# Performance work log

Hardware: AMD Instinct MI355X
Metric: run time of the kernel (lower is better)

## Reference

```python
import jax, jax.numpy as jnp
import numpy as np

EPS = 1e-5
K = 20

def knn_idx(x, k):
    # x: (B, C, N); returns indices of k nearest neighbors (incl. self), (B, N, k)
    xx = jnp.sum(x * x, axis=1, keepdims=True)            # (B,1,N)
    inner = -2.0 * jnp.einsum('bcn,bcm->bnm', x, x)       # (B,N,N)
    d = -jnp.swapaxes(xx, 1, 2) - inner - xx              # -||xi - xj||^2
    return jax.lax.top_k(d, k)[1]

def graph_feature(x, k):
    # x: (B, C, N) -> (B, 2C, N, k) with [neighbor - center, center]
    B, C, N = x.shape
    idx = knn_idx(x, k)                                   # (B,N,k)
    feat = jnp.swapaxes(x, 1, 2)                          # (B,N,C)
    nb = jax.vmap(lambda f, i: f[i])(feat, idx)           # (B,N,k,C) gather
    ctr = jnp.broadcast_to(feat[:, :, None, :], nb.shape)
    out = jnp.concatenate([nb - ctr, ctr], axis=-1)       # (B,N,k,2C)
    return jnp.transpose(out, (0, 3, 1, 2))

def bn(x, g, b, m, v):
    # inference-mode batchnorm over channel axis 1
    shape = (1, -1) + (1,) * (x.ndim - 2)
    inv = g / jnp.sqrt(v + EPS)
    return x * inv.reshape(shape) + (b - m * inv).reshape(shape)

def edge_block(x, W, g, b, m, v):
    f = graph_feature(x, K)                               # (B,2C,N,k)
    h = jnp.einsum('bcnk,oc->bonk', f, W)                 # 1x1 conv, no bias
    h = jax.nn.relu(bn(h, g, b, m, v))
    return jnp.max(h, axis=-1)                            # max over k -> (B,O,N)

def _forward(x, W1, W2, W3, W4, W5,
             g1, b1, m1, v1, g2, b2, m2, v2, g3, b3, m3, v3,
             g4, b4, m4, v4, g5, b5, m5, v5, g6, b6, m6, v6,
             g7, b7, m7, v7, L1W, L2W, L2b, L3W, L3b):
    x1 = edge_block(x, W1, g1, b1, m1, v1)                # (B,64,N)
    x2 = edge_block(x1, W2, g2, b2, m2, v2)               # (B,64,N)
    x3 = edge_block(x2, W3, g3, b3, m3, v3)               # (B,128,N)
    x4 = edge_block(x3, W4, g4, b4, m4, v4)               # (B,256,N)
    cat = jnp.concatenate([x1, x2, x3, x4], axis=1)       # (B,512,N)
    h = jnp.einsum('bcn,oc->bon', cat, W5)                # conv5 1x1
    h = jax.nn.relu(bn(h, g5, b5, m5, v5))
    h = jnp.max(h, axis=-1)                               # adaptive max pool -> (B,1024)
    h = jax.nn.relu(bn(h @ L1W.T, g6, b6, m6, v6))        # dropout = identity (eval)
    h = jax.nn.relu(bn(h @ L2W.T + L2b, g7, b7, m7, v7))
    return h @ L3W.T + L3b                                # (B, num_classes)

def _bn_params(keys, c):
    k0, k1, k2, k3 = keys
    g = jax.random.uniform(k0, (c,), jnp.float32, 0.5, 1.5)
    b = 0.1 * jax.random.normal(k1, (c,), jnp.float32)
    m = 0.1 * jax.random.normal(k2, (c,), jnp.float32)
    v = jax.random.uniform(k3, (c,), jnp.float32, 0.5, 1.5)
    return g, b, m, v

def setup_inputs() -> dict:
    key = jax.random.key(0)
    ks = jax.random.split(key, 40)
    d = {}
    d['x'] = jax.random.normal(ks[0], (8, 4, 1024), jnp.float32)
    def w(k, o, i):
        return jax.random.normal(k, (o, i), jnp.float32) * np.float32(np.sqrt(2.0 / i))
    d['W1'] = w(ks[1], 64, 8)
    d['W2'] = w(ks[2], 64, 128)
    d['W3'] = w(ks[3], 128, 128)
    d['W4'] = w(ks[4], 256, 256)
    d['W5'] = w(ks[5], 1024, 512)
    for i, c in enumerate([64, 64, 128, 256, 1024, 512, 256]):
        g, b, m, v = _bn_params(jax.random.split(ks[6 + i], 4), c)
        d[f'g{i+1}'], d[f'b{i+1}'], d[f'm{i+1}'], d[f'v{i+1}'] = g, b, m, v
    d['L1W'] = w(ks[20], 512, 1024)
    d['L2W'] = w(ks[21], 256, 512)
    d['L2b'] = 0.1 * jax.random.normal(ks[22], (256,), jnp.float32)
    d['L3W'] = w(ks[23], 8, 256)
    d['L3b'] = 0.1 * jax.random.normal(ks[24], (8,), jnp.float32)
    return d

def reference(x, W1, W2, W3, W4, W5,
              g1, b1, m1, v1, g2, b2, m2, v2, g3, b3, m3, v3,
              g4, b4, m4, v4, g5, b5, m5, v5, g6, b6, m6, v6,
              g7, b7, m7, v7, L1W, L2W, L2b, L3W, L3b):
    return _forward(x, W1, W2, W3, W4, W5,
                    g1, b1, m1, v1, g2, b2, m2, v2, g3, b3, m3, v3,
                    g4, b4, m4, v4, g5, b5, m5, v5, g6, b6, m6, v6,
                    g7, b7, m7, v7, L1W, L2W, L2b, L3W, L3b)
```

## Files before the change

kernel.cpp:

```cpp
#include <hip/hip_runtime.h>
#include <cstdint>

#define BB 8
#define NN 1024
#define KK 20
#define EPSV 1e-5f

typedef __attribute__((ext_vector_type(8))) short bf16x8;
typedef __attribute__((ext_vector_type(4))) float f32x4;

__device__ __forceinline__ unsigned fenc(float f) {
  unsigned u = __float_as_uint(f);
  return (u & 0x80000000u) ? ~u : (u | 0x80000000u);
}
__device__ __forceinline__ float fdec(unsigned u) {
  u = (u & 0x80000000u) ? (u & 0x7FFFFFFFu) : ~u;
  return __uint_as_float(u);
}
__device__ __forceinline__ unsigned short f2bf(float f) {
  unsigned u = __float_as_uint(f);
  unsigned r = u + 0x7FFFu + ((u >> 16) & 1u);
  return (unsigned short)(r >> 16);
}

template<int C>
__global__ __launch_bounds__(256) void xx_kernel(const float* __restrict__ x, float* __restrict__ xx) {
  int p = blockIdx.x * 256 + threadIdx.x;
  if (p >= BB * NN) return;
  int b = p >> 10, n = p & (NN - 1);
  const float* xb = x + (size_t)b * C * NN + n;
  float s = 0.f;
  #pragma unroll
  for (int c = 0; c < C; ++c) { float t = xb[(size_t)c * NN]; s = fmaf(t, t, s); }
  xx[p] = s;
}

template<int C>
__global__ __launch_bounds__(256) void dist_kernel(const float* __restrict__ x, const float* __restrict__ xx,
                                                   float* __restrict__ d, int b0) {
  constexpr int CC = (C < 32) ? C : 32;
  __shared__ __align__(16) float xi[CC][128];
  __shared__ __align__(16) float xj[CC][128];
  int bl = blockIdx.z, b = b0 + bl;
  int i0 = blockIdx.y * 128, j0 = blockIdx.x * 128;
  int t = threadIdx.x;
  int w = t >> 6, lane = t & 63;
  int wi = (w >> 1) * 64, wj = (w & 1) * 64;
  int li = (lane >> 3) * 8, lj = (lane & 7) * 8;
  float acc[8][8] = {};
  const float* xb = x + (size_t)b * C * NN;
  for (int c0 = 0; c0 < C; c0 += CC) {
    __syncthreads();
    for (int p = t; p < CC * 32; p += 256) {
      int cc = p >> 5, col = (p & 31) * 4;
      *reinterpret_cast<float4*>(&xi[cc][col]) =
        *reinterpret_cast<const float4*>(&xb[(size_t)(c0 + cc) * NN + i0 + col]);
      *reinterpret_cast<float4*>(&xj[cc][col]) =
        *reinterpret_cast<const float4*>(&xb[(size_t)(c0 + cc) * NN + j0 + col]);
    }
    __syncthreads();
    #pragma unroll
    for (int cc = 0; cc < CC; ++cc) {
      float4 A0 = *reinterpret_cast<const float4*>(&xi[cc][wi + li]);
      float4 A1 = *reinterpret_cast<const float4*>(&xi[cc][wi + li + 4]);
      float4 B0 = *reinterpret_cast<const float4*>(&xj[cc][wj + lj]);
      float4 B1 = *reinterpret_cast<const float4*>(&xj[cc][wj + lj + 4]);
      float av[8] = {A0.x, A0.y, A0.z, A0.w, A1.x, A1.y, A1.z, A1.w};
      float bv[8] = {B0.x, B0.y, B0.z, B0.w, B1.x, B1.y, B1.z, B1.w};
      #pragma unroll
      for (int a = 0; a < 8; ++a)
        #pragma unroll
        for (int q = 0; q < 8; ++q)
          acc[a][q] = fmaf(av[a], bv[q], acc[a][q]);
    }
  }
  float xxj[8];
  #pragma unroll
  for (int q = 0; q < 8; ++q) xxj[q] = xx[b * NN + j0 + wj + lj + q];
  #pragma unroll
  for (int a = 0; a < 8; ++a) {
    int i = i0 + wi + li + a;
    float xxi = xx[b * NN + i];
    float4 o0v, o1v;
    o0v.x = 2.f * acc[a][0] - xxi - xxj[0];
    o0v.y = 2.f * acc[a][1] - xxi - xxj[1];
    o0v.z = 2.f * acc[a][2] - xxi - xxj[2];
    o0v.w = 2.f * acc[a][3] - xxi - xxj[3];
    o1v.x = 2.f * acc[a][4] - xxi - xxj[4];
    o1v.y = 2.f * acc[a][5] - xxi - xxj[5];
    o1v.z = 2.f * acc[a][6] - xxi - xxj[6];
    o1v.w = 2.f * acc[a][7] - xxi - xxj[7];
    *reinterpret_cast<float4*>(&d[((size_t)bl * NN + i) * NN + j0 + wj + lj]) = o0v;
    *reinterpret_cast<float4*>(&d[((size_t)bl * NN + i) * NN + j0 + wj + lj + 4]) = o1v;
  }
}

__global__ __launch_bounds__(256) void topk_kernel(const float* __restrict__ d, int* __restrict__ idx, int b0) {
  int t = threadIdx.x;
  int wave = t >> 6, lane = t & 63;
  int bl = blockIdx.y, b = b0 + bl;
  int i = blockIdx.x * 4 + wave;
  const float* row = d + ((size_t)bl * NN + i) * NN;

  unsigned v[16];
  #pragma unroll
  for (int p = 0; p < 4; ++p) {
    float4 f = *reinterpret_cast<const float4*>(&row[p * 256 + lane * 4]);
    v[p * 4 + 0] = fenc(f.x);
    v[p * 4 + 1] = fenc(f.y);
    v[p * 4 + 2] = fenc(f.z);
    v[p * 4 + 3] = fenc(f.w);
  }

  unsigned long long lo = 0, hi = 0xFFFFFFFFull;
  while (lo < hi) {
    unsigned long long mid = lo + ((hi - lo + 1) >> 1);
    unsigned mt = (unsigned)mid;
    int c = 0;
    #pragma unroll
    for (int e = 0; e < 16; ++e)
      c += __popcll(__ballot(v[e] >= mt));
    if (c >= KK) lo = mid; else hi = mid - 1;
  }
  unsigned T = (unsigned)lo;

  int* op = idx + ((size_t)b * NN + i) * KK;
  int base = 0, n1 = 0;
  #pragma unroll
  for (int e = 0; e < 16; ++e) {
    unsigned long long mask = __ballot(v[e] > T);
    unsigned mb = __builtin_amdgcn_mbcnt_lo((unsigned)mask, 0u);
    mb = __builtin_amdgcn_mbcnt_hi((unsigned)(mask >> 32), mb);
    if (v[e] > T) op[base + mb] = (e >> 2) * 256 + lane * 4 + (e & 3);
    base += __popcll(mask);
  }
  n1 = base;
  int need = KK - n1;
  int neq = 0;
  #pragma unroll
  for (int e = 0; e < 16; ++e) neq += __popcll(__ballot(v[e] == T));
  if (neq == need) {
    #pragma unroll
    for (int e = 0; e < 16; ++e) {
      unsigned long long mask = __ballot(v[e] == T);
      unsigned mb = __builtin_amdgcn_mbcnt_lo((unsigned)mask, 0u);
      mb = __builtin_amdgcn_mbcnt_hi((unsigned)(mask >> 32), mb);
      if (v[e] == T) op[base + mb] = (e >> 2) * 256 + lane * 4 + (e & 3);
      base += __popcll(mask);
    }
  } else {
    unsigned taken = 0;
    for (int s = 0; s < need; ++s) {
      int jm = 1 << 30;
      #pragma unroll
      for (int e = 0; e < 16; ++e) {
        if (v[e] == T && !((taken >> e) & 1u)) {
          int j = (e >> 2) * 256 + lane * 4 + (e & 3);
          jm = jm < j ? jm : j;
        }
      }
      #pragma unroll
      for (int st = 1; st < 64; st <<= 1) {
        int oj = __shfl_xor(jm, st);
        jm = jm < oj ? jm : oj;
      }
      if (lane == ((jm >> 2) & 63)) {
        int e = (((jm >> 8) << 2) | (jm & 3));
        taken |= 1u << e;
        op[base + s] = jm;
      }
    }
  }
}

template<int C, int O>
__global__ __launch_bounds__(256) void pgemm_kernel(const float* __restrict__ x, const float* __restrict__ W,
                                                    float* __restrict__ Plo, float* __restrict__ Phi) {
  constexpr int CC = (C < 64) ? C : 64;
  __shared__ __align__(16) float xs[CC][64];
  __shared__ __align__(16) float wls[CC][68];
  __shared__ __align__(16) float whs[CC][68];
  int b = blockIdx.z;
  int o0 = blockIdx.y * 64, n0 = blockIdx.x * 64;
  int t = threadIdx.x;
  int tn = t & 15, to = t >> 4;
  float accl[4][4] = {}, acch[4][4] = {};
  const float* xb = x + (size_t)b * C * NN;
  for (int c0 = 0; c0 < C; c0 += CC) {
    __syncthreads();
    for (int p = t; p < CC * 64; p += 256) {
      int cc = p >> 6, col = p & 63;
      xs[cc][col] = xb[(size_t)(c0 + cc) * NN + n0 + col];
    }
    for (int p = t; p < 64 * CC; p += 256) {
      int ol = p / CC, cc = p % CC;
      wls[cc][ol] = W[(size_t)(o0 + ol) * (2 * C) + c0 + cc];
      whs[cc][ol] = W[(size_t)(o0 + ol) * (2 * C) + C + c0 + cc];
    }
    __syncthreads();
    #pragma unroll
    for (int cc = 0; cc < CC; ++cc) {
      float4 X  = *reinterpret_cast<const float4*>(&xs[cc][tn * 4]);
      float4 Wl = *reinterpret_cast<const float4*>(&wls[cc][to * 4]);
      float4 Wh = *reinterpret_cast<const float4*>(&whs[cc][to * 4]);
      float xv[4] = {X.x, X.y, X.z, X.w};
      float wl[4] = {Wl.x, Wl.y, Wl.z, Wl.w};
      float wh[4] = {Wh.x, Wh.y, Wh.z, Wh.w};
      #pragma unroll
      for (int a = 0; a < 4; ++a)
        #pragma unroll
        for (int q = 0; q < 4; ++q) {
          accl[a][q] = fmaf(wl[a], xv[q], accl[a][q]);
          acch[a][q] = fmaf(wh[a], xv[q], acch[a][q]);
        }
    }
  }
  #pragma unroll
  for (int a = 0; a < 4; ++a) {
    int o = o0 + to * 4 + a;
    size_t base = ((size_t)b * O + o) * NN + n0 + tn * 4;
    float4 vl = {accl[a][0], accl[a][1], accl[a][2], accl[a][3]};
    float4 vh = {acch[a][0], acch[a][1], acch[a][2], acch[a][3]};
    *reinterpret_cast<float4*>(&Plo[base]) = vl;
    *reinterpret_cast<float4*>(&Phi[base]) = vh;
  }
}

__global__ __launch_bounds__(256) void edgemax_kernel(const float* __restrict__ Plo, const float* __restrict__ Phi,
    const int* __restrict__ idx, const float* __restrict__ g, const float* __restrict__ bt,
    const float* __restrict__ m, const float* __restrict__ v,
    float* __restrict__ xout, int O) {
  __shared__ __align__(16) float srow[2][NN];
  __shared__ __align__(16) float sphi[2][64];
  __shared__ int   sidx[64 * KK];
  __shared__ float sinv[32], ssb[32];
  int b = blockIdx.z, n0 = blockIdx.y * 64, o0 = blockIdx.x * 32;
  int t = threadIdx.x;
  if (t < 32) {
    float inv = g[o0 + t] / sqrtf(v[o0 + t] + EPSV);
    sinv[t] = inv; ssb[t] = bt[o0 + t] - m[o0 + t] * inv;
  }
  for (int p = t; p < 64 * KK; p += 256) sidx[p] = idx[((size_t)b * NN + n0) * KK + p];
  const float* plobase = Plo + (size_t)b * O * NN;
  const float* phibase = Phi + (size_t)b * O * NN;
  float4 cur0 = *reinterpret_cast<const float4*>(&plobase[(size_t)(o0 + 0) * NN + t * 4]);
  float4 cur1 = *reinterpret_cast<const float4*>(&plobase[(size_t)(o0 + 1) * NN + t * 4]);
  float4 curphi;
  if (t < 32) curphi = *reinterpret_cast<const float4*>(&phibase[(size_t)(o0 + (t >> 4)) * NN + n0 + (t & 15) * 4]);
  __syncthreads();
  int n = t >> 2, kg = t & 3;
  int j0 = sidx[n * KK + kg * 5 + 0];
  int j1 = sidx[n * KK + kg * 5 + 1];
  int j2 = sidx[n * KK + kg * 5 + 2];
  int j3 = sidx[n * KK + kg * 5 + 3];
  int j4 = sidx[n * KK + kg * 5 + 4];
  for (int oo = 0; oo < 32; oo += 2) {
    *reinterpret_cast<float4*>(&srow[0][t * 4]) = cur0;
    *reinterpret_cast<float4*>(&srow[1][t * 4]) = cur1;
    if (t < 32) *reinterpret_cast<float4*>(&sphi[t >> 4][(t & 15) * 4]) = curphi;
    if (oo < 30) {
      cur0 = *reinterpret_cast<const float4*>(&plobase[(size_t)(o0 + oo + 2) * NN + t * 4]);
      cur1 = *reinterpret_cast<const float4*>(&plobase[(size_t)(o0 + oo + 3) * NN + t * 4]);
      if (t < 32) curphi = *reinterpret_cast<const float4*>(&phibase[(size_t)(o0 + oo + 2 + (t >> 4)) * NN + n0 + (t & 15) * 4]);
    }
    __syncthreads();
    float mx0 = srow[0][j0];
    mx0 = fmaxf(mx0, srow[0][j1]);
    mx0 = fmaxf(mx0, srow[0][j2]);
    mx0 = fmaxf(mx0, srow[0][j3]);
    mx0 = fmaxf(mx0, srow[0][j4]);
    float mx1 = srow[1][j0];
    mx1 = fmaxf(mx1, srow[1][j1]);
    mx1 = fmaxf(mx1, srow[1][j2]);
    mx1 = fmaxf(mx1, srow[1][j3]);
    mx1 = fmaxf(mx1, srow[1][j4]);
    mx0 = fmaxf(mx0, __shfl_xor(mx0, 1));
    mx0 = fmaxf(mx0, __shfl_xor(mx0, 2));
    mx1 = fmaxf(mx1, __shfl_xor(mx1, 1));
    mx1 = fmaxf(mx1, __shfl_xor(mx1, 2));
    if (kg == 0) {
      float z0 = mx0 - srow[0][n0 + n] + sphi[0][n];
      float z1 = mx1 - srow[1][n0 + n] + sphi[1][n];
      xout[((size_t)b * O + o0 + oo) * NN + n0 + n]     = fmaxf(fmaf(z0, sinv[oo],     ssb[oo]),     0.f);
      xout[((size_t)b * O + o0 + oo + 1) * NN + n0 + n] = fmaxf(fmaf(z1, sinv[oo + 1], ssb[oo + 1]), 0.f);
    }
    __syncthreads();
  }
}

__global__ __launch_bounds__(256) void tcvt_kernel(const float* __restrict__ src,
    unsigned short* __restrict__ dst, int Csrc, int c0) {
  __shared__ float tile[64][65];
  int b = blockIdx.z, cb = blockIdx.y * 64, n0 = blockIdx.x * 64;
  int t = threadIdx.x;
  const float* s = src + ((size_t)b * Csrc + cb) * NN + n0;
  #pragma unroll
  for (int rr = 0; rr < 4; ++rr) {
    int r = (t >> 4) + rr * 16;
    float4 v = *reinterpret_cast<const float4*>(&s[(size_t)r * NN + (t & 15) * 4]);
    tile[r][(t & 15) * 4 + 0] = v.x;
    tile[r][(t & 15) * 4 + 1] = v.y;
    tile[r][(t & 15) * 4 + 2] = v.z;
    tile[r][(t & 15) * 4 + 3] = v.w;
  }
  __syncthreads();
  #pragma unroll
  for (int rr = 0; rr < 2; ++rr) {
    int chunk = t + 256 * rr;
    int n = chunk >> 3, cg = (chunk & 7) * 8;
    unsigned short u[8];
    #pragma unroll
    for (int j = 0; j < 8; ++j) u[j] = f2bf(tile[cg + j][n]);
    *reinterpret_cast<uint4*>(&dst[((size_t)b * NN + n0 + n) * 512 + c0 + cb + cg]) =
      *reinterpret_cast<const uint4*>(u);
  }
}

__global__ __launch_bounds__(256) void cvtw_kernel(const float* __restrict__ W, unsigned short* __restrict__ Wb) {
  int p = (blockIdx.x * 256 + threadIdx.x) * 4;
  float4 v = *reinterpret_cast<const float4*>(&W[p]);
  unsigned short u[4] = {f2bf(v.x), f2bf(v.y), f2bf(v.z), f2bf(v.w)};
  *reinterpret_cast<uint2*>(&Wb[p]) = *reinterpret_cast<const uint2*>(u);
}

__global__ __launch_bounds__(256) void pgemm4_mfma_kernel(const unsigned short* __restrict__ Xb,
    const unsigned short* __restrict__ W4b, float* __restrict__ Plo_t, float* __restrict__ Phi_t) {
  int b = blockIdx.z;
  int n0 = blockIdx.x * 128, o0 = blockIdx.y * 64;
  int t = threadIdx.x, lane = t & 63, w = t >> 6;
  int r = lane & 15, kc = lane >> 4;
  const unsigned short* A  = Xb + ((size_t)b * NN + n0 + w * 32 + r) * 512 + 128 + kc * 8;
  const unsigned short* Bw = W4b + ((size_t)(o0 + r)) * 256 + kc * 8;
  f32x4 accl0[4] = {}, accl1[4] = {}, acch0[4] = {}, acch1[4] = {};
  #pragma unroll
  for (int ks = 0; ks < 128; ks += 32) {
    bf16x8 a0 = *reinterpret_cast<const bf16x8*>(A + ks);
    bf16x8 a1 = *reinterpret_cast<const bf16x8*>(A + 16 * 512 + ks);
    #pragma unroll
    for (int j = 0; j < 4; ++j) {
      bf16x8 bl = *reinterpret_cast<const bf16x8*>(Bw + (size_t)j * 16 * 256 + ks);
      bf16x8 bh = *reinterpret_cast<const bf16x8*>(Bw + (size_t)j * 16 * 256 + 128 + ks);
      accl0[j] = __builtin_amdgcn_mfma_f32_16x16x32_bf16(a0, bl, accl0[j], 0, 0, 0);
      accl1[j] = __builtin_amdgcn_mfma_f32_16x16x32_bf16(a1, bl, accl1[j], 0, 0, 0);
      acch0[j] = __builtin_amdgcn_mfma_f32_16x16x32_bf16(a0, bh, acch0[j], 0, 0, 0);
      acch1[j] = __builtin_amdgcn_mfma_f32_16x16x32_bf16(a1, bh, acch1[j], 0, 0, 0);
    }
  }
  #pragma unroll
  for (int j = 0; j < 4; ++j) {
    #pragma unroll
    for (int reg = 0; reg < 4; ++reg) {
      size_t n_a = (size_t)b * NN + n0 + w * 32 + kc * 4 + reg;
      size_t n_b = n_a + 16;
      int oc = o0 + j * 16 + r;
      Plo_t[n_a * 256 + oc] = accl0[j][reg];
      Plo_t[n_b * 256 + oc] = accl1[j][reg];
      Phi_t[n_a * 256 + oc] = acch0[j][reg];
      Phi_t[n_b * 256 + oc] = acch1[j][reg];
    }
  }
}

__global__ __launch_bounds__(256) void edgemax4_kernel(const float* __restrict__ Plo_t,
    const float* __restrict__ Phi_t, const int* __restrict__ idx,
    const float* __restrict__ g, const float* __restrict__ bt,
    const float* __restrict__ m, const float* __restrict__ v,
    unsigned short* __restrict__ Xb) {
  int b = blockIdx.y, t = threadIdx.x;
  int n = blockIdx.x * 4 + (t >> 6);
  int oc = (t & 63) * 4;
  const int* ip = idx + ((size_t)b * NN + n) * KK;
  const float* base = Plo_t + (size_t)b * NN * 256;
  float4 mx = {-3.4e38f, -3.4e38f, -3.4e38f, -3.4e38f};
  #pragma unroll
  for (int k = 0; k < KK; ++k) {
    float4 vv = *reinterpret_cast<const float4*>(base + (size_t)ip[k] * 256 + oc);
    mx.x = fmaxf(mx.x, vv.x);
    mx.y = fmaxf(mx.y, vv.y);
    mx.z = fmaxf(mx.z, vv.z);
    mx.w = fmaxf(mx.w, vv.w);
  }
  float4 self = *reinterpret_cast<const float4*>(base + (size_t)n * 256 + oc);
  float4 ph = *reinterpret_cast<const float4*>(Phi_t + ((size_t)b * NN + n) * 256 + oc);
  float4 gg = *reinterpret_cast<const float4*>(g + oc);
  float4 bb = *reinterpret_cast<const float4*>(bt + oc);
  float4 mm = *reinterpret_cast<const float4*>(m + oc);
  float4 vv4 = *reinterpret_cast<const float4*>(v + oc);
  float mxa[4] = {mx.x, mx.y, mx.z, mx.w};
  float sfa[4] = {self.x, self.y, self.z, self.w};
  float pha[4] = {ph.x, ph.y, ph.z, ph.w};
  float ga[4] = {gg.x, gg.y, gg.z, gg.w};
  float ba[4] = {bb.x, bb.y, bb.z, bb.w};
  float ma[4] = {mm.x, mm.y, mm.z, mm.w};
  float va[4] = {vv4.x, vv4.y, vv4.z, vv4.w};
  unsigned short u[4];
  #pragma unroll
  for (int e = 0; e < 4; ++e) {
    float inv = ga[e] / sqrtf(va[e] + EPSV);
    float z = mxa[e] - sfa[e] + pha[e];
    float y = fmaxf(fmaf(z, inv, ba[e] - ma[e] * inv), 0.f);
    u[e] = f2bf(y);
  }
  *reinterpret_cast<uint2*>(&Xb[((size_t)b * NN + n) * 512 + 256 + oc]) =
    *reinterpret_cast<const uint2*>(u);
}

__global__ __launch_bounds__(256) void conv5_mfma_kernel(const unsigned short* __restrict__ Xb,
    const unsigned short* __restrict__ W5b, unsigned* __restrict__ henc) {
  int b = blockIdx.z;
  int n0 = blockIdx.x * 128, o0 = blockIdx.y * 64;
  int t = threadIdx.x, lane = t & 63, w = t >> 6;
  int r = lane & 15, kc = lane >> 4;
  const unsigned short* A = W5b + ((size_t)(o0 + r)) * 512 + kc * 8;
  const unsigned short* B = Xb + ((size_t)b * NN + n0 + w * 32 + r) * 512 + kc * 8;
  f32x4 acc00 = {}, acc01 = {}, acc10 = {}, acc11 = {};
  f32x4 acc20 = {}, acc21 = {}, acc30 = {}, acc31 = {};
  bf16x8 a0 = *reinterpret_cast<const bf16x8*>(A + 0 * 16 * 512);
  bf16x8 a1 = *reinterpret_cast<const bf16x8*>(A + 1 * 16 * 512);
  bf16x8 a2 = *reinterpret_cast<const bf16x8*>(A + 2 * 16 * 512);
  bf16x8 a3 = *reinterpret_cast<const bf16x8*>(A + 3 * 16 * 512);
  bf16x8 b0 = *reinterpret_cast<const bf16x8*>(B);
  bf16x8 b1 = *reinterpret_cast<const bf16x8*>(B + 16 * 512);
  #pragma unroll
  for (int ks = 0; ks < 512; ks += 32) {
    bf16x8 na0, na1, na2, na3, nb0, nb1;
    if (ks + 32 < 512) {
      na0 = *reinterpret_cast<const bf16x8*>(A + 0 * 16 * 512 + ks + 32);
      na1 = *reinterpret_cast<const bf16x8*>(A + 1 * 16 * 512 + ks + 32);
      na2 = *reinterpret_cast<const bf16x8*>(A + 2 * 16 * 512 + ks + 32);
      na3 = *reinterpret_cast<const bf16x8*>(A + 3 * 16 * 512 + ks + 32);
      nb0 = *reinterpret_cast<const bf16x8*>(B + ks + 32);
      nb1 = *reinterpret_cast<const bf16x8*>(B + 16 * 512 + ks + 32);
    }
    acc00 = __builtin_amdgcn_mfma_f32_16x16x32_bf16(a0, b0, acc00, 0, 0, 0);
    acc01 = __builtin_amdgcn_mfma_f32_16x16x32_bf16(a0, b1, acc01, 0, 0, 0);
    acc10 = __builtin_amdgcn_mfma_f32_16x16x32_bf16(a1, b0, acc10, 0, 0, 0);
    acc11 = __builtin_amdgcn_mfma_f32_16x16x32_bf16(a1, b1, acc11, 0, 0, 0);
    acc20 = __builtin_amdgcn_mfma_f32_16x16x32_bf16(a2, b0, acc20, 0, 0, 0);
    acc21 = __builtin_amdgcn_mfma_f32_16x16x32_bf16(a2, b1, acc21, 0, 0, 0);
    acc30 = __builtin_amdgcn_mfma_f32_16x16x32_bf16(a3, b0, acc30, 0, 0, 0);
    acc31 = __builtin_amdgcn_mfma_f32_16x16x32_bf16(a3, b1, acc31, 0, 0, 0);
    a0 = na0; a1 = na1; a2 = na2; a3 = na3; b0 = nb0; b1 = nb1;
  }
  f32x4 m0 = {fmaxf(acc00[0], acc01[0]), fmaxf(acc00[1], acc01[1]),
              fmaxf(acc00[2], acc01[2]), fmaxf(acc00[3], acc01[3])};
  f32x4 m1 = {fmaxf(acc10[0], acc11[0]), fmaxf(acc10[1], acc11[1]),
              fmaxf(acc10[2], acc11[2]), fmaxf(acc10[3], acc11[3])};
  f32x4 m2 = {fmaxf(acc20[0], acc21[0]), fmaxf(acc20[1], acc21[1]),
              fmaxf(acc20[2], acc21[2]), fmaxf(acc20[3], acc21[3])};
  f32x4 m3 = {fmaxf(acc30[0], acc31[0]), fmaxf(acc30[1], acc31[1]),
              fmaxf(acc30[2], acc31[2]), fmaxf(acc30[3], acc31[3])};
  #pragma unroll
  for (int st = 1; st < 16; st <<= 1) {
    #pragma unroll
    for (int reg = 0; reg < 4; ++reg) {
      m0[reg] = fmaxf(m0[reg], __shfl_xor(m0[reg], st));
      m1[reg] = fmaxf(m1[reg], __shfl_xor(m1[reg], st));
      m2[reg] = fmaxf(m2[reg], __shfl_xor(m2[reg], st));
      m3[reg] = fmaxf(m3[reg], __shfl_xor(m3[reg], st));
    }
  }
  if (r == 0) {
    #pragma unroll
    for (int reg = 0; reg < 4; ++reg) {
      atomicMax(&henc[b * 1024 + o0 + 0 * 16 + kc * 4 + reg], fenc(m0[reg]));
      atomicMax(&henc[b * 1024 + o0 + 1 * 16 + kc * 4 + reg], fenc(m1[reg]));
      atomicMax(&henc[b * 1024 + o0 + 2 * 16 + kc * 4 + reg], fenc(m2[reg]));
      atomicMax(&henc[b * 1024 + o0 + 3 * 16 + kc * 4 + reg], fenc(m3[reg]));
    }
  }
}

__global__ __launch_bounds__(256) void fc1_kernel(
    const unsigned* __restrict__ henc,
    const float* __restrict__ g5, const float* __restrict__ b5, const float* __restrict__ m5, const float* __restrict__ v5,
    const float* __restrict__ L1W,
    const float* __restrict__ g6, const float* __restrict__ b6, const float* __restrict__ m6, const float* __restrict__ v6,
    float* __restrict__ y1) {
  __shared__ float sh[1024];
  int b = blockIdx.y, t = threadIdx.x;
  int o0 = blockIdx.x * 64;
  for (int o = t; o < 1024; o += 256) {
    float f = fdec(henc[b * 1024 + o]);
    float inv = g5[o] / sqrtf(v5[o] + EPSV);
    sh[o] = fmaxf(fmaf(f, inv, b5[o] - m5[o] * inv), 0.f);
  }
  __syncthreads();
  int o = o0 + (t >> 2), part = t & 3;
  float acc = 0.f;
  const float4* w4 = reinterpret_cast<const float4*>(L1W + (size_t)o * 1024 + part * 256);
  const float4* h4 = reinterpret_cast<const float4*>(sh + part * 256);
  #pragma unroll 8
  for (int c = 0; c < 64; ++c) {
    float4 a = w4[c], q = h4[c];
    acc = fmaf(a.x, q.x, fmaf(a.y, q.y, fmaf(a.z, q.z, fmaf(a.w, q.w, acc))));
  }
  acc += __shfl_xor(acc, 1);
  acc += __shfl_xor(acc, 2);
  if (part == 0) {
    float inv = g6[o] / sqrtf(v6[o] + EPSV);
    y1[b * 512 + o] = fmaxf(fmaf(acc, inv, b6[o] - m6[o] * inv), 0.f);
  }
}

__global__ __launch_bounds__(256) void fc2_kernel(
    const float* __restrict__ y1,
    const float* __restrict__ L2W, const float* __restrict__ L2b,
    const float* __restrict__ g7, const float* __restrict__ b7, const float* __restrict__ m7, const float* __restrict__ v7,
    const float* __restrict__ L3W, const float* __restrict__ L3b,
    float* __restrict__ out) {
  __shared__ float sy1[512];
  __shared__ float sy2[256];
  int b = blockIdx.x, t = threadIdx.x;
  for (int o = t; o < 512; o += 256) sy1[o] = y1[b * 512 + o];
  __syncthreads();
  {
    int o = t;
    float acc = L2b[o];
    const float4* w4 = reinterpret_cast<const float4*>(L2W + (size_t)o * 512);
    const float4* q4 = reinterpret_cast<const float4*>(sy1);
    for (int c = 0; c < 128; ++c) {
      float4 a = w4[c], q = q4[c];
      acc = fmaf(a.x, q.x, fmaf(a.y, q.y, fmaf(a.z, q.z, fmaf(a.w, q.w, acc))));
    }
    float inv = g7[o] / sqrtf(v7[o] + EPSV);
    sy2[o] = fmaxf(fmaf(acc, inv, b7[o] - m7[o] * inv), 0.f);
  }
  __syncthreads();
  if (t < 8) {
    float acc = L3b[t];
    const float4* w4 = reinterpret_cast<const float4*>(L3W + (size_t)t * 256);
    const float4* q4 = reinterpret_cast<const float4*>(sy2);
    for (int c = 0; c < 64; ++c) {
      float4 a = w4[c], q = q4[c];
      acc = fmaf(a.x, q.x, fmaf(a.y, q.y, fmaf(a.z, q.z, fmaf(a.w, q.w, acc))));
    }
    out[b * 8 + t] = acc;
  }
}

extern "C" void kernel_launch(void* const* d_in, const int* in_sizes, int n_in,
                              void* d_out, int out_size, void* d_ws, size_t ws_size,
                              hipStream_t stream) {
  (void)in_sizes; (void)n_in; (void)out_size;
  const float* x   = (const float*)d_in[0];
  const float* W1  = (const float*)d_in[1];
  const float* W2  = (const float*)d_in[2];
  const float* W3  = (const float*)d_in[3];
  const float* W4  = (const float*)d_in[4];
  const float* W5  = (const float*)d_in[5];
  const float* bnp[7][4];
  for (int i = 0; i < 7; ++i)
    for (int j = 0; j < 4; ++j)
      bnp[i][j] = (const float*)d_in[6 + i * 4 + j];
  const float* L1W = (const float*)d_in[34];
  const float* L2W = (const float*)d_in[35];
  const float* L2b = (const float*)d_in[36];
  const float* L3W = (const float*)d_in[37];
  const float* L3b = (const float*)d_in[38];
  float* out = (float*)d_out;

  char* wsb = (char*)d_ws;
  size_t off = 0;
  auto alloc = [&](size_t bytes) -> void* {
    void* p = wsb + off; off += (bytes + 255) & ~(size_t)255; return p;
  };
  int*      idx  = (int*)     alloc((size_t)BB * NN * KK * 4);
  float*    xx   = (float*)   alloc((size_t)BB * NN * 4);
  float*    x1   = (float*)   alloc((size_t)BB * 64  * NN * 4);
  float*    x2   = (float*)   alloc((size_t)BB * 64  * NN * 4);
  float*    x3   = (float*)   alloc((size_t)BB * 128 * NN * 4);
  float*    Plo  = (float*)   alloc((size_t)BB * 256 * NN * 4);
  float*    Phi  = (float*)   alloc((size_t)BB * 256 * NN * 4);
  unsigned* henc = (unsigned*)alloc((size_t)BB * 1024 * 4);
  float*    y1   = (float*)   alloc((size_t)BB * 512 * 4);
  unsigned short* Xb  = (unsigned short*)alloc((size_t)BB * NN * 512 * 2);
  unsigned short* W5b = (unsigned short*)alloc((size_t)1024 * 512 * 2);
  unsigned short* W4b = (unsigned short*)alloc((size_t)256 * 256 * 2);
  size_t left = (ws_size > off) ? (ws_size - off) : 0;
  int nb = 8;
  while (nb > 1 && (size_t)nb * NN * NN * 4 > left) nb >>= 1;
  float* dbuf = (float*)(wsb + off);

  dim3 thr(256);
  #define KNN_PHASE(CIN, XIN)                                                              \
    xx_kernel<CIN><<<dim3(32), thr, 0, stream>>>(XIN, xx);                                 \
    for (int b0 = 0; b0 < BB; b0 += nb) {                                                  \
      dist_kernel<CIN><<<dim3(8, 8, nb), thr, 0, stream>>>(XIN, xx, dbuf, b0);             \
      topk_kernel<<<dim3(NN / 4, nb), thr, 0, stream>>>(dbuf, idx, b0);                    \
    }

  cvtw_kernel<<<dim3(512), thr, 0, stream>>>(W5, W5b);
  cvtw_kernel<<<dim3(64), thr, 0, stream>>>(W4, W4b);

  KNN_PHASE(4, x)
  pgemm_kernel<4, 64><<<dim3(16, 1, BB), thr, 0, stream>>>(x, W1, Plo, Phi);
  edgemax_kernel<<<dim3(2, 16, BB), thr, 0, stream>>>(Plo, Phi, idx,
      bnp[0][0], bnp[0][1], bnp[0][2], bnp[0][3], x1, 64);
  tcvt_kernel<<<dim3(16, 1, BB), thr, 0, stream>>>(x1, Xb, 64, 0);
  KNN_PHASE(64, x1)
  pgemm_kernel<64, 64><<<dim3(16, 1, BB), thr, 0, stream>>>(x1, W2, Plo, Phi);
  edgemax_kernel<<<dim3(2, 16, BB), thr, 0, stream>>>(Plo, Phi, idx,
      bnp[1][0], bnp[1][1], bnp[1][2], bnp[1][3], x2, 64);
  tcvt_kernel<<<dim3(16, 1, BB), thr, 0, stream>>>(x2, Xb, 64, 64);
  KNN_PHASE(64, x2)
  pgemm_kernel<64, 128><<<dim3(16, 2, BB), thr, 0, stream>>>(x2, W3, Plo, Phi);
  edgemax_kernel<<<dim3(4, 16, BB), thr, 0, stream>>>(Plo, Phi, idx,
      bnp[2][0], bnp[2][1], bnp[2][2], bnp[2][3], x3, 128);
  tcvt_kernel<<<dim3(16, 2, BB), thr, 0, stream>>>(x3, Xb, 128, 128);
  KNN_PHASE(128, x3)
  pgemm4_mfma_kernel<<<dim3(8, 4, BB), thr, 0, stream>>>(Xb, W4b, Plo, Phi);
  edgemax4_kernel<<<dim3(256, BB), thr, 0, stream>>>(Plo, Phi, idx,
      bnp[3][0], bnp[3][1], bnp[3][2], bnp[3][3], Xb);
  #undef KNN_PHASE

  hipMemsetAsync(henc, 0, (size_t)BB * 1024 * 4, stream);
  conv5_mfma_kernel<<<dim3(8, 16, BB), thr, 0, stream>>>(Xb, W5b, henc);

  fc1_kernel<<<dim3(8, BB), thr, 0, stream>>>(henc,
      bnp[4][0], bnp[4][1], bnp[4][2], bnp[4][3], L1W,
      bnp[5][0], bnp[5][1], bnp[5][2], bnp[5][3], y1);
  fc2_kernel<<<dim3(BB), thr, 0, stream>>>(y1,
      L2W, L2b, bnp[6][0], bnp[6][1], bnp[6][2], bnp[6][3], L3W, L3b, out);
}
```

Baseline: 464.1 us.

## Fuse distance computation and top-k into single kNN kernel without global distance matrix

Replaces the separate distance-matrix kernel and top-k kernel with one kernel per 8 query rows. Each thread computes distances to 4 candidate points, packs the value and index into a 64-bit key, runs a per-wave binary-search selection, and merges the per-wave candidates in shared memory. This removes writing and re-reading the full N×N distance buffer in global memory, at the cost of lower arithmetic reuse (each block re-reads all of x) and longer 42-bit binary searches. Ties are broken by lower index through the key encoding.

Measured after the change: 600.0 us. 1.29x slower.

```diff
diff --git a/kernel.cpp b/kernel.cpp
--- a/kernel.cpp
+++ b/kernel.cpp
@@ -21,6 +21,10 @@
   unsigned u = __float_as_uint(f);
   unsigned r = u + 0x7FFFu + ((u >> 16) & 1u);
   return (unsigned short)(r >> 16);
+}
+__device__ __forceinline__ unsigned mbcnt64(unsigned long long m) {
+  unsigned r = __builtin_amdgcn_mbcnt_lo((unsigned)m, 0u);
+  return __builtin_amdgcn_mbcnt_hi((unsigned)(m >> 32), r);
 }
 
 template<int C>
@@ -36,140 +40,87 @@
 }
 
 template<int C>
-__global__ __launch_bounds__(256) void dist_kernel(const float* __restrict__ x, const float* __restrict__ xx,
-                                                   float* __restrict__ d, int b0) {
-  constexpr int CC = (C < 32) ? C : 32;
-  __shared__ __align__(16) float xi[CC][128];
-  __shared__ __align__(16) float xj[CC][128];
-  int bl = blockIdx.z, b = b0 + bl;
-  int i0 = blockIdx.y * 128, j0 = blockIdx.x * 128;
-  int t = threadIdx.x;
-  int w = t >> 6, lane = t & 63;
-  int wi = (w >> 1) * 64, wj = (w & 1) * 64;
-  int li = (lane >> 3) * 8, lj = (lane & 7) * 8;
-  float acc[8][8] = {};
+__global__ __launch_bounds__(256) void knn_kernel(const float* __restrict__ x, const float* __restrict__ xx,
+                                                  int* __restrict__ idx) {
+  __shared__ float xit[C][8];
+  __shared__ float sxxi[8];
+  __shared__ unsigned long long cand[8][80];
+  int b = blockIdx.y;
+  int i0 = blockIdx.x * 8;
+  int t = threadIdx.x, lane = t & 63, w = t >> 6;
   const float* xb = x + (size_t)b * C * NN;
-  for (int c0 = 0; c0 < C; c0 += CC) {
-    __syncthreads();
-    for (int p = t; p < CC * 32; p += 256) {
-      int cc = p >> 5, col = (p & 31) * 4;
-      *reinterpret_cast<float4*>(&xi[cc][col]) =
-        *reinterpret_cast<const float4*>(&xb[(size_t)(c0 + cc) * NN + i0 + col]);
-      *reinterpret_cast<float4*>(&xj[cc][col]) =
-        *reinterpret_cast<const float4*>(&xb[(size_t)(c0 + cc) * NN + j0 + col]);
-    }
-    __syncthreads();
-    #pragma unroll
-    for (int cc = 0; cc < CC; ++cc) {
-      float4 A0 = *reinterpret_cast<const float4*>(&xi[cc][wi + li]);
-      float4 A1 = *reinterpret_cast<const float4*>(&xi[cc][wi + li + 4]);
-      float4 B0 = *reinterpret_cast<const float4*>(&xj[cc][wj + lj]);
-      float4 B1 = *reinterpret_cast<const float4*>(&xj[cc][wj + lj + 4]);
-      float av[8] = {A0.x, A0.y, A0.z, A0.w, A1.x, A1.y, A1.z, A1.w};
-      float bv[8] = {B0.x, B0.y, B0.z, B0.w, B1.x, B1.y, B1.z, B1.w};
+  for (int p = t; p < C * 8; p += 256)
+    xit[p >> 3][p & 7] = xb[(size_t)(p >> 3) * NN + i0 + (p & 7)];
+  if (t < 8) sxxi[t] = xx[b * NN + i0 + t];
+  __syncthreads();
+
+  float acc[8][4] = {};
+  float4 xxj4 = *reinterpret_cast<const float4*>(&xx[b * NN + t * 4]);
+  #pragma unroll 4
+  for (int c = 0; c < C; ++c) {
+    float4 xj = *reinterpret_cast<const float4*>(&xb[(size_t)c * NN + t * 4]);
+    float4 xiA = *reinterpret_cast<const float4*>(&xit[c][0]);
+    float4 xiB = *reinterpret_cast<const float4*>(&xit[c][4]);
+    float xr[8] = {xiA.x, xiA.y, xiA.z, xiA.w, xiB.x, xiB.y, xiB.z, xiB.w};
+    float xjv[4] = {xj.x, xj.y, xj.z, xj.w};
+    #pragma unroll
+    for (int r = 0; r < 8; ++r)
       #pragma unroll
-      for (int a = 0; a < 8; ++a)
-        #pragma unroll
-        for (int q = 0; q < 8; ++q)
-          acc[a][q] = fmaf(av[a], bv[q], acc[a][q]);
-    }
-  }
-  float xxj[8];
-  #pragma unroll
-  for (int q = 0; q < 8; ++q) xxj[q] = xx[b * NN + j0 + wj + lj + q];
-  #pragma unroll
-  for (int a = 0; a < 8; ++a) {
-    int i = i0 + wi + li + a;
-    float xxi = xx[b * NN + i];
-    float4 o0v, o1v;
-    o0v.x = 2.f * acc[a][0] - xxi - xxj[0];
-    o0v.y = 2.f * acc[a][1] - xxi - xxj[1];
-    o0v.z = 2.f * acc[a][2] - xxi - xxj[2];
-    o0v.w = 2.f * acc[a][3] - xxi - xxj[3];
-    o1v.x = 2.f * acc[a][4] - xxi - xxj[4];
-    o1v.y = 2.f * acc[a][5] - xxi - xxj[5];
-    o1v.z = 2.f * acc[a][6] - xxi - xxj[6];
-    o1v.w = 2.f * acc[a][7] - xxi - xxj[7];
-    *reinterpret_cast<float4*>(&d[((size_t)bl * NN + i) * NN + j0 + wj + lj]) = o0v;
-    *reinterpret_cast<float4*>(&d[((size_t)bl * NN + i) * NN + j0 + wj + lj + 4]) = o1v;
-  }
-}
-
-__global__ __launch_bounds__(256) void topk_kernel(const float* __restrict__ d, int* __restrict__ idx, int b0) {
-  int t = threadIdx.x;
-  int wave = t >> 6, lane = t & 63;
-  int bl = blockIdx.y, b = b0 + bl;
-  int i = blockIdx.x * 4 + wave;
-  const float* row = d + ((size_t)bl * NN + i) * NN;
-
-  unsigned v[16];
-  #pragma unroll
-  for (int p = 0; p < 4; ++p) {
-    float4 f = *reinterpret_cast<const float4*>(&row[p * 256 + lane * 4]);
-    v[p * 4 + 0] = fenc(f.x);
-    v[p * 4 + 1] = fenc(f.y);
-    v[p * 4 + 2] = fenc(f.z);
-    v[p * 4 + 3] = fenc(f.w);
-  }
-
-  unsigned long long lo = 0, hi = 0xFFFFFFFFull;
-  while (lo < hi) {
-    unsigned long long mid = lo + ((hi - lo + 1) >> 1);
-    unsigned mt = (unsigned)mid;
-    int c = 0;
-    #pragma unroll
-    for (int e = 0; e < 16; ++e)
-      c += __popcll(__ballot(v[e] >= mt));
-    if (c >= KK) lo = mid; else hi = mid - 1;
-  }
-  unsigned T = (unsigned)lo;
-
-  int* op = idx + ((size_t)b * NN + i) * KK;
-  int base = 0, n1 = 0;
-  #pragma unroll
-  for (int e = 0; e < 16; ++e) {
-    unsigned long long mask = __ballot(v[e] > T);
-    unsigned mb = __builtin_amdgcn_mbcnt_lo((unsigned)mask, 0u);
-    mb = __builtin_amdgcn_mbcnt_hi((unsigned)(mask >> 32), mb);
-    if (v[e] > T) op[base + mb] = (e >> 2) * 256 + lane * 4 + (e & 3);
-    base += __popcll(mask);
-  }
-  n1 = base;
-  int need = KK - n1;
-  int neq = 0;
-  #pragma unroll
-  for (int e = 0; e < 16; ++e) neq += __popcll(__ballot(v[e] == T));
-  if (neq == need) {
-    #pragma unroll
-    for (int e = 0; e < 16; ++e) {
-      unsigned long long mask = __ballot(v[e] == T);
-      unsigned mb = __builtin_amdgcn_mbcnt_lo((unsigned)mask, 0u);
-      mb = __builtin_amdgcn_mbcnt_hi((unsigned)(mask >> 32), mb);
-      if (v[e] == T) op[base + mb] = (e >> 2) * 256 + lane * 4 + (e & 3);
+      for (int q = 0; q < 4; ++q)
+        acc[r][q] = fmaf(xr[r], xjv[q], acc[r][q]);
+  }
+
+  unsigned long long key[8][4];
+  float xxjv[4] = {xxj4.x, xxj4.y, xxj4.z, xxj4.w};
+  #pragma unroll
+  for (int r = 0; r < 8; ++r) {
+    float xxi = sxxi[r];
+    #pragma unroll
+    for (int q = 0; q < 4; ++q) {
+      float dv = 2.f * acc[r][q] - xxi - xxjv[q];
+      key[r][q] = ((unsigned long long)fenc(dv) << 10) | (unsigned)(1023 - (t * 4 + q));
+    }
+  }
+
+  #pragma unroll
+  for (int r = 0; r < 8; ++r) {
+    unsigned long long lo = 0, hi = (1ull << 42) - 1;
+    while (lo < hi) {
+      unsigned long long mid = lo + ((hi - lo + 1) >> 1);
+      int cnt = __popcll(__ballot(key[r][0] >= mid)) + __popcll(__ballot(key[r][1] >= mid))
+              + __popcll(__ballot(key[r][2] >= mid)) + __popcll(__ballot(key[r][3] >= mid));
+      if (cnt >= KK) lo = mid; else hi = mid - 1;
+    }
+    int base = 0;
+    #pragma unroll
+    for (int q = 0; q < 4; ++q) {
+      unsigned long long mask = __ballot(key[r][q] >= lo);
+      unsigned mb = mbcnt64(mask);
+      if (key[r][q] >= lo) cand[r][w * 20 + base + mb] = key[r][q];
       base += __popcll(mask);
     }
-  } else {
-    unsigned taken = 0;
-    for (int s = 0; s < need; ++s) {
-      int jm = 1 << 30;
-      #pragma unroll
-      for (int e = 0; e < 16; ++e) {
-        if (v[e] == T && !((taken >> e) & 1u)) {
-          int j = (e >> 2) * 256 + lane * 4 + (e & 3);
-          jm = jm < j ? jm : j;
-        }
-      }
-      #pragma unroll
-      for (int st = 1; st < 64; st <<= 1) {
-        int oj = __shfl_xor(jm, st);
-        jm = jm < oj ? jm : oj;
-      }
-      if (lane == ((jm >> 2) & 63)) {
-        int e = (((jm >> 8) << 2) | (jm & 3));
-        taken |= 1u << e;
-        op[base + s] = jm;
-      }
-    }
+  }
+  __syncthreads();
+
+  #pragma unroll
+  for (int rr = 0; rr < 2; ++rr) {
+    int r = w + rr * 4;
+    unsigned long long ka = cand[r][lane];
+    unsigned long long kb = (lane < 16) ? cand[r][64 + lane] : 0ull;
+    unsigned long long lo = 0, hi = (1ull << 42) - 1;
+    while (lo < hi) {
+      unsigned long long mid = lo + ((hi - lo + 1) >> 1);
+      int cnt = __popcll(__ballot(ka >= mid)) + __popcll(__ballot(kb >= mid));
+      if (cnt >= KK) lo = mid; else hi = mid - 1;
+    }
+    int* op = idx + ((size_t)b * NN + i0 + r) * KK;
+    unsigned long long mask_a = __ballot(ka >= lo);
+    unsigned mba = mbcnt64(mask_a);
+    if (ka >= lo) op[mba] = 1023 - (int)(ka & 1023u);
+    int base = __popcll(mask_a);
+    unsigned long long mask_b = __ballot(kb >= lo);
+    unsigned mbb = mbcnt64(mask_b);
+    if (kb >= lo) op[base + mbb] = 1023 - (int)(kb & 1023u);
   }
 }
 
@@ -542,7 +493,7 @@
 extern "C" void kernel_launch(void* const* d_in, const int* in_sizes, int n_in,
                               void* d_out, int out_size, void* d_ws, size_t ws_size,
                               hipStream_t stream) {
-  (void)in_sizes; (void)n_in; (void)out_size;
+  (void)in_sizes; (void)n_in; (void)out_size; (void)ws_size;
   const float* x   = (const float*)d_in[0];
   const float* W1  = (const float*)d_in[1];
   const float* W2  = (const float*)d_in[2];
@@ -577,18 +528,11 @@
   unsigned short* Xb  = (unsigned short*)alloc((size_t)BB * NN * 512 * 2);
   unsigned short* W5b = (unsigned short*)alloc((size_t)1024 * 512 * 2);
   unsigned short* W4b = (unsigned short*)alloc((size_t)256 * 256 * 2);
-  size_t left = (ws_size > off) ? (ws_size - off) : 0;
-  int nb = 8;
-  while (nb > 1 && (size_t)nb * NN * NN * 4 > left) nb >>= 1;
-  float* dbuf = (float*)(wsb + off);
 
   dim3 thr(256);
   #define KNN_PHASE(CIN, XIN)                                                              \
     xx_kernel<CIN><<<dim3(32), thr, 0, stream>>>(XIN, xx);                                 \
-    for (int b0 = 0; b0 < BB; b0 += nb) {                                                  \
-      dist_kernel<CIN><<<dim3(8, 8, nb), thr, 0, stream>>>(XIN, xx, dbuf, b0);             \
-      topk_kernel<<<dim3(NN / 4, nb), thr, 0, stream>>>(dbuf, idx, b0);                    \
-    }
+    knn_kernel<CIN><<<dim3(NN / 8, BB), thr, 0, stream>>>(XIN, xx, idx);
 
   cvtw_kernel<<<dim3(512), thr, 0, stream>>>(W5, W5b);
   cvtw_kernel<<<dim3(64), thr, 0, stream>>>(W4, W4b);
```
